# Performance work log

Measured on AMD Instinct MI355X. Metric: run time of the kernel, lower is better.

Reference implementation:

```python
import jax, jax.numpy as jnp
import numpy as np

EPS = 1e-5

def _silu(x):
    return x * jax.nn.sigmoid(x)

def _layernorm(x, g, b):
    mu = jnp.mean(x, axis=-1, keepdims=True)
    var = jnp.mean((x - mu) ** 2, axis=-1, keepdims=True)
    return (x - mu) * jax.lax.rsqrt(var + EPS) * g + b

def _mamba(x, in_w, conv_w, conv_b, xproj_w, dt_w, dt_b, A_log, Dp, out_w):
    # x: (B, L, dm); faithful mamba-ssm block: in_proj -> causal dwconv -> silu ->
    # x_proj -> softplus(dt_proj) -> selective scan -> gate -> out_proj
    B, L, dm = x.shape
    di, K = conv_w.shape          # d_inner, d_conv
    ds = A_log.shape[1]           # d_state
    dtr = dt_w.shape[1]           # dt_rank
    xz = x @ in_w.T               # (B, L, 2*di)
    xi, z = jnp.split(xz, 2, axis=-1)
    # causal depthwise conv1d (pad K-1 on the left), kernel unrolled (K=4)
    xpad = jnp.pad(xi, ((0, 0), (K - 1, 0), (0, 0)))
    xc = conv_b + sum(conv_w[:, k] * xpad[:, k:k + L, :] for k in range(K))
    xc = _silu(xc)                # (B, L, di)
    xdbl = xc @ xproj_w.T         # (B, L, dtr + 2*ds)
    dt, Bm, Cm = jnp.split(xdbl, [dtr, dtr + ds], axis=-1)
    delta = jax.nn.softplus(dt @ dt_w.T + dt_b)        # (B, L, di)
    A = -jnp.exp(A_log)                                # (di, ds)
    dA = jnp.exp(delta[..., None] * A)                 # (B, L, di, ds)
    dBu = delta[..., None] * Bm[:, :, None, :] * xc[..., None]
    def step(h, inp):
        dA_t, dBu_t, C_t = inp                         # (B,di,ds),(B,di,ds),(B,ds)
        h = dA_t * h + dBu_t
        y = jnp.einsum('bdn,bn->bd', h, C_t)
        return h, y
    h0 = jnp.zeros((B, di, ds), dtype=x.dtype)
    _, ys = jax.lax.scan(step, h0, (dA.transpose(1, 0, 2, 3),
                                    dBu.transpose(1, 0, 2, 3),
                                    Cm.transpose(1, 0, 2)))
    y = ys.transpose(1, 0, 2) + xc * Dp                # (B, L, di)
    y = y * _silu(z)
    return y @ out_w.T                                 # (B, L, dm)

def _forward(t1, t2, t3, t4, t5,
             m0_in_w, m0_conv_w, m0_conv_b, m0_xproj_w, m0_dt_w, m0_dt_b, m0_Alog, m0_D, m0_out_w,
             m1_in_w, m1_conv_w, m1_conv_b, m1_xproj_w, m1_dt_w, m1_dt_b, m1_Alog, m1_D, m1_out_w,
             norm_g, norm_b, proj_w, proj_b, norm1_g, norm1_b, proj1_w, proj1_b, skip_scale):
    B = t1.shape[0]
    flat = lambda t, c: t.reshape(B, c, -1).transpose(0, 2, 1)   # (B, N, C)
    f1, f2, f3, f4, f5 = flat(t1, 8), flat(t2, 16), flat(t3, 24), flat(t4, 32), flat(t5, 48)
    c1 = jnp.concatenate([f1[:, :, 0:8], f2[:, :, 0:8], f3[:, :, 0:8], f4[:, :, 0:8], f5[:, :, 0:8]], axis=1)   # (B,21824,8)
    c2 = jnp.concatenate([f2[:, :, 8:16], f3[:, :, 8:16], f4[:, :, 8:16], f5[:, :, 8:16]], axis=1)              # (B,5440,8)
    c3 = jnp.concatenate([f3[:, :, 16:24], f4[:, :, 16:24], f5[:, :, 16:24]], axis=1)                           # (B,1344,8)
    c4 = jnp.concatenate([f4[:, :, 24:32], f5[:, :, 24:32]], axis=1)                                            # (B,320,8)
    c5 = f5[:, :, 32:48]                                                                                        # (B,64,16)
    def block8(c):
        y = _mamba(c, m0_in_w, m0_conv_w, m0_conv_b, m0_xproj_w, m0_dt_w, m0_dt_b, m0_Alog, m0_D, m0_out_w)
        return _layernorm(y + skip_scale * c, norm_g, norm_b) @ proj_w.T + proj_b
    x1m, x2m, x3m, x4m = block8(c1), block8(c2), block8(c3), block8(c4)
    y5 = _mamba(c5, m1_in_w, m1_conv_w, m1_conv_b, m1_xproj_w, m1_dt_w, m1_dt_b, m1_Alog, m1_D, m1_out_w)
    x5m = _layernorm(y5 + skip_scale * c5, norm1_g, norm1_b) @ proj1_w.T + proj1_b
    a1 = x1m[:, 0:16384, :]
    a2 = jnp.concatenate([x1m[:, 16384:20480, :], x2m[:, 0:4096, :]], axis=2)
    a3 = jnp.concatenate([x1m[:, 20480:21504, :], x2m[:, 4096:5120, :], x3m[:, 0:1024, :]], axis=2)
    a4 = jnp.concatenate([x1m[:, 21504:21760, :], x2m[:, 5120:5376, :], x3m[:, 1024:1280, :], x4m[:, 0:256, :]], axis=2)
    a5 = jnp.concatenate([x1m[:, 21760:, :], x2m[:, 5376:, :], x3m[:, 1280:, :], x4m[:, 256:, :], x5m], axis=2)
    x1 = a1.transpose(0, 2, 1).reshape(B, 8, 128, 128)
    x2 = a2.transpose(0, 2, 1).reshape(B, 16, 64, 64)
    x3 = a3.transpose(0, 2, 1).reshape(B, 24, 32, 32)
    x4 = a4.transpose(0, 2, 1).reshape(B, 32, 16, 16)
    x5 = a5.transpose(0, 2, 1).reshape(B, 48, 8, 8)
    return (x1, x2, x3, x4, x5)

def setup_inputs() -> dict:
    key = jax.random.key(0)
    ks = iter(jax.random.split(key, 64))
    B = 8
    def n(shape, s=1.0):
        return jax.random.normal(next(ks), shape, dtype=jnp.float32) * s
    inp = {
        't1': n((B, 8, 128, 128)), 't2': n((B, 16, 64, 64)), 't3': n((B, 24, 32, 32)),
        't4': n((B, 32, 16, 16)), 't5': n((B, 48, 8, 8)),
    }
    def mamba_params(pfx, dm):
        di, ds, K, dtr = 2 * dm, 16, 4, 1  # expand=2, d_state=16, d_conv=4, dt_rank=ceil(dm/16)=1
        return {
            pfx + '_in_w': n((2 * di, dm), dm ** -0.5),
            pfx + '_conv_w': n((di, K), 0.3),
            pfx + '_conv_b': n((di,), 0.1),
            pfx + '_xproj_w': n((dtr + 2 * ds, di), di ** -0.5),
            pfx + '_dt_w': n((di, dtr), 1.0),
            pfx + '_dt_b': n((di,), 0.1) - 3.0,
            pfx + '_Alog': jnp.log(jnp.tile(jnp.arange(1.0, ds + 1.0, dtype=jnp.float32), (di, 1))),
            pfx + '_D': jnp.ones((di,), jnp.float32),
            pfx + '_out_w': n((dm, di), di ** -0.5),
        }
    inp.update(mamba_params('m0', 8))
    inp.update(mamba_params('m1', 16))
    inp.update({
        'norm_g': jnp.ones((8,), jnp.float32), 'norm_b': jnp.zeros((8,), jnp.float32),
        'proj_w': n((8, 8), 8 ** -0.5), 'proj_b': jnp.zeros((8,), jnp.float32),
        'norm1_g': jnp.ones((16,), jnp.float32), 'norm1_b': jnp.zeros((16,), jnp.float32),
        'proj1_w': n((16, 16), 16 ** -0.5), 'proj1_b': jnp.zeros((16,), jnp.float32),
        'skip_scale': jnp.ones((1,), jnp.float32),
    })
    return inp

def reference(t1, t2, t3, t4, t5,
              m0_in_w, m0_conv_w, m0_conv_b, m0_xproj_w, m0_dt_w, m0_dt_b, m0_Alog, m0_D, m0_out_w,
              m1_in_w, m1_conv_w, m1_conv_b, m1_xproj_w, m1_dt_w, m1_dt_b, m1_Alog, m1_D, m1_out_w,
              norm_g, norm_b, proj_w, proj_b, norm1_g, norm1_b, proj1_w, proj1_b, skip_scale):
    return _forward(t1, t2, t3, t4, t5,
                    m0_in_w, m0_conv_w, m0_conv_b, m0_xproj_w, m0_dt_w, m0_dt_b, m0_Alog, m0_D, m0_out_w,
                    m1_in_w, m1_conv_w, m1_conv_b, m1_xproj_w, m1_dt_w, m1_dt_b, m1_Alog, m1_D, m1_out_w,
                    norm_g, norm_b, proj_w, proj_b, norm1_g, norm1_b, proj1_w, proj1_b, skip_scale)
```

## Files before the change

### kernel.cpp

```cpp
#include <hip/hip_runtime.h>
#include <cmath>

#define SCH 128
#define SUB 32
#define NCB 228
#define NCHUNK 1824
#define NSUB 7296
#define LOG2E 1.442695041f
#define LN2F  0.6931471806f
#define EXP2F(x) __builtin_exp2f(x)
#define LOG2F(x) __builtin_log2f(x)
#define SW_IN 0
#define SW_CONVW 256
#define SW_CONVB 320
#define SW_XPROJ 336
#define SW_DTW 864
#define SW_DTB 880
#define SW_A 896
#define SW_D 1152
#define SW_OUTW 1168
#define SW_NG 1296
#define SW_NB 1304
#define SW_PW 1312
#define SW_PB 1376
#define SW_SKIP 1384
#define REC 1392
#define RSTR 25
#define GR_C 3200
#define GR_X8 4224
#define GRECW 4736
#define SMEMP1 4592
#define C3 4592
#define X83 5616
#define YOF 6128
#define V_IN 0
#define V_CONVW 1024
#define V_CONVB 1152
#define V_XPROJ 1184
#define V_DTW 2240
#define V_DTB 2272
#define V_A 2304
#define V_D 2816
#define V_OUTW 2848
#define V_NG 3360
#define V_NB 3376
#define V_PW 3392
#define V_PB 3648
#define V_SKIP 3664
#define V_XC 3668
#define V_DL 5780
#define V_BM 7892
#define V_CM 8916
#define SMEM3 9940

struct Params {
  const float *t0, *t1, *t2, *t3, *t4;
  const float *in_w0,*conv_w0,*conv_b0,*xproj0,*dtw0,*dtb0,*Alog0,*D0,*outw0;
  const float *in_w1,*conv_w1,*conv_b1,*xproj1,*dtw1,*dtb1,*Alog1,*D1,*outw1;
  const float *ng,*nb,*pw,*pb,*n1g,*n1b,*p1w,*p1b,*skip;
  float* out;
  float *hloc, *sumdelta, *grec;
};

__device__ __forceinline__ float softplusf(float x) {
  float t = EXP2F(-fabsf(x) * LOG2E);
  return fmaxf(x, 0.f) + LOG2F(1.f + t) * LN2F;
}
__device__ __forceinline__ float siluf(float x) { return x * (1.f / (1.f + __expf(-x))); }
__device__ __forceinline__ unsigned pk(float a, float b) {
  unsigned ua = __float_as_uint(a) + 0x8000u;
  unsigned ub = __float_as_uint(b) + 0x8000u;
  return (ua >> 16) | (ub & 0xFFFF0000u);
}
__device__ __forceinline__ float lo16(unsigned w) { return __uint_as_float(w << 16); }
__device__ __forceinline__ float hi16(unsigned w) { return __uint_as_float(w & 0xFFFF0000u); }

struct Loc { int k, pos, ch, hw, C; };

__device__ __forceinline__ Loc locate(int seq, int l) {
  Loc r;
  if (seq == 0) { r.ch = 0;
    if (l < 16384)      { r.k=0; r.pos=l;        r.hw=16384; r.C=8;  }
    else if (l < 20480) { r.k=1; r.pos=l-16384;  r.hw=4096;  r.C=16; }
    else if (l < 21504) { r.k=2; r.pos=l-20480;  r.hw=1024;  r.C=24; }
    else if (l < 21760) { r.k=3; r.pos=l-21504;  r.hw=256;   r.C=32; }
    else                { r.k=4; r.pos=l-21760;  r.hw=64;    r.C=48; }
  } else if (seq == 1) { r.ch = 8;
    if (l < 4096)       { r.k=1; r.pos=l;        r.hw=4096;  r.C=16; }
    else if (l < 5120)  { r.k=2; r.pos=l-4096;   r.hw=1024;  r.C=24; }
    else if (l < 5376)  { r.k=3; r.pos=l-5120;   r.hw=256;   r.C=32; }
    else                { r.k=4; r.pos=l-5376;   r.hw=64;    r.C=48; }
  } else if (seq == 2) { r.ch = 16;
    if (l < 1024)       { r.k=2; r.pos=l;        r.hw=1024;  r.C=24; }
    else if (l < 1280)  { r.k=3; r.pos=l-1024;   r.hw=256;   r.C=32; }
    else                { r.k=4; r.pos=l-1280;   r.hw=64;    r.C=48; }
  } else { r.ch = 24;
    if (l < 256)        { r.k=3; r.pos=l;        r.hw=256;   r.C=32; }
    else                { r.k=4; r.pos=l-256;    r.hw=64;    r.C=48; }
  }
  return r;
}

__device__ __forceinline__ const float* tsel(const Params& p, int k) {
  switch (k) { case 0: return p.t0; case 1: return p.t1; case 2: return p.t2;
               case 3: return p.t3; default: return p.t4; }
}
__device__ __forceinline__ int outbase(int k) {
  switch (k) { case 0: return 0; case 1: return 1048576; case 2: return 1572864;
               case 3: return 1769472; default: return 1835008; }
}

__device__ __forceinline__ void gather8(const Params& p, int b, int seq, int l, float* c) {
  Loc lc = locate(seq, l);
  const float* t = tsel(p, lc.k);
  int base = (b * lc.C + lc.ch) * lc.hw + lc.pos;
  #pragma unroll
  for (int j = 0; j < 8; ++j) c[j] = t[base + j * lc.hw];
}

__device__ __forceinline__ void decode_bid(int bid, int& b, int& seq, int& l0, int& Sa) {
  b = bid / NCB;
  int r = bid - b * NCB;
  int c, L;
  if (r < 171)      { seq = 0; c = r;       L = 21824; }
  else if (r < 214) { seq = 1; c = r - 171; L = 5440;  }
  else if (r < 225) { seq = 2; c = r - 214; L = 1344;  }
  else              { seq = 3; c = r - 225; L = 320;   }
  l0 = c * SCH;
  int rem = L - l0;
  Sa = rem < SCH ? rem : SCH;
}

__device__ void load_w0(const Params& p, float* s, int tid) {
  for (int i = tid; i < 256; i += 256) s[SW_IN + i] = p.in_w0[i];
  for (int i = tid; i < 64;  i += 256) s[SW_CONVW + i] = p.conv_w0[i];
  for (int i = tid; i < 16;  i += 256) s[SW_CONVB + i] = p.conv_b0[i];
  for (int i = tid; i < 528; i += 256) s[SW_XPROJ + i] = p.xproj0[i];
  for (int i = tid; i < 16;  i += 256) s[SW_DTW + i] = p.dtw0[i];
  for (int i = tid; i < 16;  i += 256) s[SW_DTB + i] = p.dtb0[i];
  for (int i = tid; i < 256; i += 256) s[SW_A + i] = -__expf(p.Alog0[i]) * LOG2E;
  for (int i = tid; i < 16;  i += 256) s[SW_D + i] = p.D0[i];
  for (int i = tid; i < 128; i += 256) s[SW_OUTW + i] = p.outw0[i];
  for (int i = tid; i < 8;   i += 256) s[SW_NG + i] = p.ng[i];
  for (int i = tid; i < 8;   i += 256) s[SW_NB + i] = p.nb[i];
  for (int i = tid; i < 64;  i += 256) s[SW_PW + i] = p.pw[i];
  for (int i = tid; i < 8;   i += 256) s[SW_PB + i] = p.pb[i];
  if (tid == 0) s[SW_SKIP] = p.skip[0];
}

__device__ __forceinline__ float dot16h(const float* w, int ch0, int cho,
                                        const float* a, const float* o) {
  float4 wa0 = *(const float4*)&w[ch0];
  float4 wa1 = *(const float4*)&w[ch0 + 4];
  float4 wb0 = *(const float4*)&w[cho];
  float4 wb1 = *(const float4*)&w[cho + 4];
  float r = wa0.x * a[0];
  r = fmaf(wa0.y, a[1], r); r = fmaf(wa0.z, a[2], r); r = fmaf(wa0.w, a[3], r);
  r = fmaf(wa1.x, a[4], r); r = fmaf(wa1.y, a[5], r);
  r = fmaf(wa1.z, a[6], r); r = fmaf(wa1.w, a[7], r);
  r = fmaf(wb0.x, o[0], r); r = fmaf(wb0.y, o[1], r);
  r = fmaf(wb0.z, o[2], r); r = fmaf(wb0.w, o[3], r);
  r = fmaf(wb1.x, o[4], r); r = fmaf(wb1.y, o[5], r);
  r = fmaf(wb1.z, o[6], r); r = fmaf(wb1.w, o[7], r);
  return r;
}

__global__ __launch_bounds__(256, 8) void k_pass1(Params p) {
  __shared__ float s[SMEMP1];
  int tid = threadIdx.x;
  int cid = blockIdx.x;
  int b, seq, l0, Sa;
  decode_bid(cid, b, seq, l0, Sa);
  int tok = tid >> 1, hf = tid & 1;
  int ch0 = hf * 8, cho = 8 - ch0;
  bool act = tok < Sa;
  bool grow = tok < Sa + 3;
  bool hrow = (Sa == SCH) && (tok >= SCH - 3);
  unsigned* gc = (unsigned*)(p.grec + (size_t)cid * GRECW);
  float x8[8], x8h[8];
  {
    int l = l0 - 3 + tok;
    if (grow && l >= 0) gather8(p, b, seq, l, x8);
    else {
      #pragma unroll
      for (int j = 0; j < 8; ++j) x8[j] = 0.f;
    }
  }
  if (hrow) gather8(p, b, seq, l0 + tok, x8h);
  load_w0(p, s, tid);
  if (hf == 0) {
    if (grow && tok >= 3) {
      uint4 v = make_uint4(pk(x8[0], x8[1]), pk(x8[2], x8[3]),
                           pk(x8[4], x8[5]), pk(x8[6], x8[7]));
      *(uint4*)&gc[GR_X8 + (tok - 3) * 4] = v;
    }
    if (hrow) {
      uint4 v = make_uint4(pk(x8h[0], x8h[1]), pk(x8h[2], x8h[3]),
                           pk(x8h[4], x8h[5]), pk(x8h[6], x8h[7]));
      *(uint4*)&gc[GR_X8 + tok * 4] = v;
    }
  }
  __syncthreads();
  if (grow) {
    #pragma unroll
    for (int ii = 0; ii < 8; ++ii) {
      int i = ch0 + ii;
      float4 wa = *(const float4*)&s[SW_IN + i * 8];
      float4 wb = *(const float4*)&s[SW_IN + i * 8 + 4];
      float a = wa.x * x8[0];
      a = fmaf(wa.y, x8[1], a); a = fmaf(wa.z, x8[2], a); a = fmaf(wa.w, x8[3], a);
      a = fmaf(wb.x, x8[4], a); a = fmaf(wb.y, x8[5], a);
      a = fmaf(wb.z, x8[6], a); a = fmaf(wb.w, x8[7], a);
      s[REC + tok * 17 + i] = a;
    }
  }
  if (hrow) {
    int r = tok + 3;
    #pragma unroll
    for (int ii = 0; ii < 8; ++ii) {
      int i = ch0 + ii;
      float4 wa = *(const float4*)&s[SW_IN + i * 8];
      float4 wb = *(const float4*)&s[SW_IN + i * 8 + 4];
      float a = wa.x * x8h[0];
      a = fmaf(wa.y, x8h[1], a); a = fmaf(wa.z, x8h[2], a); a = fmaf(wa.w, x8h[3], a);
      a = fmaf(wb.x, x8h[4], a); a = fmaf(wb.y, x8h[5], a);
      a = fmaf(wb.z, x8h[6], a); a = fmaf(wb.w, x8h[7], a);
      s[REC + r * 17 + i] = a;
    }
  }
  __syncthreads();
  float xc8[8], xco[8];
  float dt = 0.f;
  if (act) {
    #pragma unroll
    for (int ii = 0; ii < 8; ++ii) {
      int i = ch0 + ii;
      float4 cw = *(const float4*)&s[SW_CONVW + i * 4];
      float a = s[SW_CONVB + i];
      a = fmaf(cw.x, s[REC + (tok + 0) * 17 + i], a);
      a = fmaf(cw.y, s[REC + (tok + 1) * 17 + i], a);
      a = fmaf(cw.z, s[REC + (tok + 2) * 17 + i], a);
      a = fmaf(cw.w, s[REC + (tok + 3) * 17 + i], a);
      xc8[ii] = siluf(a);
    }
    #pragma unroll
    for (int ii = 0; ii < 8; ++ii) xco[ii] = __shfl_xor(xc8[ii], 1);
    dt = dot16h(&s[SW_XPROJ], ch0, cho, xc8, xco);
  }
  __syncthreads();
  unsigned* ru = (unsigned*)&s[REC + tok * RSTR];
  if (act) {
    #pragma unroll
    for (int q = 0; q < 4; ++q) {
      int d0 = ch0 + 2 * q;
      float da = softplusf(fmaf(dt, s[SW_DTW + d0],     s[SW_DTB + d0]));
      float db = softplusf(fmaf(dt, s[SW_DTW + d0 + 1], s[SW_DTB + d0 + 1]));
      ru[hf * 4 + q]     = pk(da, db);
      ru[8 + hf * 4 + q] = pk(xc8[2*q], xc8[2*q + 1]);
    }
    #pragma unroll
    for (int q = 0; q < 4; ++q) {
      int n0 = ch0 + 2 * q;
      float a0 = dot16h(&s[SW_XPROJ + (1 + n0) * 16], ch0, cho, xc8, xco);
      float a1 = dot16h(&s[SW_XPROJ + (2 + n0) * 16], ch0, cho, xc8, xco);
      ru[16 + hf * 4 + q] = pk(a0, a1);
    }
    uint4 cv;
    {
      int n0 = ch0;
      float a0 = dot16h(&s[SW_XPROJ + (17 + n0) * 16], ch0, cho, xc8, xco);
      float a1 = dot16h(&s[SW_XPROJ + (18 + n0) * 16], ch0, cho, xc8, xco);
      float a2 = dot16h(&s[SW_XPROJ + (19 + n0) * 16], ch0, cho, xc8, xco);
      float a3 = dot16h(&s[SW_XPROJ + (20 + n0) * 16], ch0, cho, xc8, xco);
      float a4 = dot16h(&s[SW_XPROJ + (21 + n0) * 16], ch0, cho, xc8, xco);
      float a5 = dot16h(&s[SW_XPROJ + (22 + n0) * 16], ch0, cho, xc8, xco);
      float a6 = dot16h(&s[SW_XPROJ + (23 + n0) * 16], ch0, cho, xc8, xco);
      float a7 = dot16h(&s[SW_XPROJ + (24 + n0) * 16], ch0, cho, xc8, xco);
      cv = make_uint4(pk(a0, a1), pk(a2, a3), pk(a4, a5), pk(a6, a7));
    }
    *(uint4*)&gc[GR_C + tok * 8 + hf * 4] = cv;
  } else {
    #pragma unroll
    for (int q = 0; q < 4; ++q) {
      ru[hf * 4 + q] = 0u;
      ru[8 + hf * 4 + q] = 0u;
      ru[16 + hf * 4 + q] = 0u;
    }
    *(uint4*)&gc[GR_C + tok * 8 + hf * 4] = make_uint4(0u, 0u, 0u, 0u);
  }
  __syncthreads();
  const unsigned* su = (const unsigned*)s;
  {
    uint4* g4 = (uint4*)gc;
    const uint4* s4 = (const uint4*)&su[REC];
    #pragma unroll 2
    for (int i4 = tid; i4 < GR_C / 4; i4 += 256) g4[i4] = s4[i4];
  }
  int w = tid >> 6, lane = tid & 63;
  int d = lane >> 2, ng = lane & 3;
  int dh = d >> 1;
  bool dodd = d & 1;
  int t0 = w * SUB;
  float4 Av = *(float4*)&s[SW_A + d * 16 + ng * 4];
  float h0 = 0.f, h1 = 0.f, h2 = 0.f, h3 = 0.f, sd = 0.f;
  for (int tile = 0; tile < 8; ++tile) {
    int tb = t0 + tile * 4;
    unsigned wd[4], wx[4]; uint2 wB[4];
    #pragma unroll
    for (int i = 0; i < 4; ++i) {
      int base = REC + (tb + i) * RSTR;
      wd[i] = su[base + dh];
      wx[i] = su[base + 8 + dh];
      wB[i] = *(const uint2*)&su[base + 16 + ng * 2];
    }
    #pragma unroll
    for (int i = 0; i < 4; ++i) {
      float dl = dodd ? hi16(wd[i]) : lo16(wd[i]);
      float u = dl * (dodd ? hi16(wx[i]) : lo16(wx[i]));
      float e0 = EXP2F(Av.x * dl), e1 = EXP2F(Av.y * dl);
      float e2 = EXP2F(Av.z * dl), e3 = EXP2F(Av.w * dl);
      h0 = fmaf(e0, h0, u * lo16(wB[i].x));
      h1 = fmaf(e1, h1, u * hi16(wB[i].x));
      h2 = fmaf(e2, h2, u * lo16(wB[i].y));
      h3 = fmaf(e3, h3, u * hi16(wB[i].y));
      sd += dl;
    }
  }
  int gs = cid * 4 + w;
  unsigned* hu = (unsigned*)p.hloc;
  hu[gs * 128 + d * 8 + ng * 2]     = pk(h0, h1);
  hu[gs * 128 + d * 8 + ng * 2 + 1] = pk(h2, h3);
  if (ng == 0) p.sumdelta[(size_t)gs * 16 + d] = sd;
}

__device__ void load_w1(const Params& p, float* s, int tid) {
  for (int i = tid; i < 1024; i += 256) s[V_IN + i] = p.in_w1[i];
  for (int i = tid; i < 128;  i += 256) s[V_CONVW + i] = p.conv_w1[i];
  for (int i = tid; i < 32;   i += 256) s[V_CONVB + i] = p.conv_b1[i];
  for (int i = tid; i < 1056; i += 256) s[V_XPROJ + i] = p.xproj1[i];
  for (int i = tid; i < 32;   i += 256) s[V_DTW + i] = p.dtw1[i];
  for (int i = tid; i < 32;   i += 256) s[V_DTB + i] = p.dtb1[i];
  for (int i = tid; i < 512;  i += 256) s[V_A + i] = -__expf(p.Alog1[i]) * LOG2E;
  for (int i = tid; i < 32;   i += 256) s[V_D + i] = p.D1[i];
  for (int i = tid; i < 512;  i += 256) s[V_OUTW + i] = p.outw1[i];
  for (int i = tid; i < 16;   i += 256) s[V_NG + i] = p.n1g[i];
  for (int i = tid; i < 16;   i += 256) s[V_NB + i] = p.n1b[i];
  for (int i = tid; i < 256;  i += 256) s[V_PW + i] = p.p1w[i];
  for (int i = tid; i < 16;   i += 256) s[V_PB + i] = p.p1b[i];
  if (tid == 0) s[V_SKIP] = p.skip[0];
}

__device__ void c5_path(const Params& p, float* s, int b, int tid) {
  load_w1(p, s, tid);
  int og = tid >> 6, tok = tid & 63;
  float x16[16];
  #pragma unroll
  for (int j = 0; j < 16; ++j) x16[j] = p.t4[(b * 48 + 32 + j) * 64 + tok];
  __syncthreads();
  #pragma unroll
  for (int ii = 0; ii < 8; ++ii) {
    int i = og * 8 + ii;
    float a = 0.f;
    #pragma unroll
    for (int j = 0; j < 16; ++j) a = fmaf(s[V_IN + i * 16 + j], x16[j], a);
    float xm1 = __shfl_up(a, 1);
    float xm2 = __shfl_up(a, 2);
    float xm3 = __shfl_up(a, 3);
    float c = s[V_CONVB + i];
    c = fmaf(s[V_CONVW + i * 4 + 3], a, c);
    if (tok >= 1) c = fmaf(s[V_CONVW + i * 4 + 2], xm1, c);
    if (tok >= 2) c = fmaf(s[V_CONVW + i * 4 + 1], xm2, c);
    if (tok >= 3) c = fmaf(s[V_CONVW + i * 4 + 0], xm3, c);
    s[V_XC + tok * 33 + i] = siluf(c);
  }
  __syncthreads();
  float xcr[32];
  #pragma unroll
  for (int i = 0; i < 32; ++i) xcr[i] = s[V_XC + tok * 33 + i];
  float dt = 0.f;
  #pragma unroll
  for (int i = 0; i < 32; ++i) dt = fmaf(s[V_XPROJ + i], xcr[i], dt);
  #pragma unroll
  for (int nn = 0; nn < 4; ++nn) {
    int n = og * 4 + nn;
    float aB = 0.f, aC = 0.f;
    #pragma unroll
    for (int i = 0; i < 32; ++i) {
      aB = fmaf(s[V_XPROJ + (1 + n) * 32 + i], xcr[i], aB);
      aC = fmaf(s[V_XPROJ + (17 + n) * 32 + i], xcr[i], aC);
    }
    s[V_BM + tok * 16 + n] = aB;
    s[V_CM + tok * 16 + n] = aC;
  }
  #pragma unroll
  for (int ii = 0; ii < 8; ++ii) {
    int d = og * 8 + ii;
    s[V_DL + tok * 33 + d] = softplusf(fmaf(dt, s[V_DTW + d], s[V_DTB + d]));
  }
  __syncthreads();
  if (tid < 128) {
    int d = tid >> 2, ng = tid & 3;
    float4 Av = *(float4*)&s[V_A + d * 16 + ng * 4];
    float h0 = 0.f, h1 = 0.f, h2 = 0.f, h3 = 0.f;
    for (int tile = 0; tile < 16; ++tile) {
      int tb = tile * 4;
      float dl[4], xv[4]; float4 bm[4], cm[4];
      #pragma unroll
      for (int i = 0; i < 4; ++i) {
        dl[i] = s[V_DL + (tb + i) * 33 + d];
        xv[i] = s[V_XC + (tb + i) * 33 + d];
        bm[i] = *(float4*)&s[V_BM + (tb + i) * 16 + ng * 4];
        cm[i] = *(float4*)&s[V_CM + (tb + i) * 16 + ng * 4];
      }
      float yp[4];
      #pragma unroll
      for (int i = 0; i < 4; ++i) {
        float u = dl[i] * xv[i];
        float e0 = EXP2F(Av.x * dl[i]), e1 = EXP2F(Av.y * dl[i]);
        float e2 = EXP2F(Av.z * dl[i]), e3 = EXP2F(Av.w * dl[i]);
        h0 = fmaf(e0, h0, u * bm[i].x);
        h1 = fmaf(e1, h1, u * bm[i].y);
        h2 = fmaf(e2, h2, u * bm[i].z);
        h3 = fmaf(e3, h3, u * bm[i].w);
        float y = h0 * cm[i].x;
        y = fmaf(h1, cm[i].y, y); y = fmaf(h2, cm[i].z, y); y = fmaf(h3, cm[i].w, y);
        yp[i] = y;
      }
      #pragma unroll
      for (int i = 0; i < 4; ++i) yp[i] += __shfl_xor(yp[i], 1);
      #pragma unroll
      for (int i = 0; i < 4; ++i) yp[i] += __shfl_xor(yp[i], 2);
      float ysel = ng == 0 ? yp[0] : ng == 1 ? yp[1] : ng == 2 ? yp[2] : yp[3];
      s[V_DL + (tb + ng) * 33 + d] = ysel;
    }
  }
  __syncthreads();
  #pragma unroll
  for (int ii = 0; ii < 8; ++ii) {
    int d = og * 8 + ii;
    float z = 0.f;
    #pragma unroll
    for (int j = 0; j < 16; ++j) z = fmaf(s[V_IN + (32 + d) * 16 + j], x16[j], z);
    float yv = (s[V_DL + tok * 33 + d] + s[V_XC + tok * 33 + d] * s[V_D + d]) * siluf(z);
    s[V_DL + tok * 33 + d] = yv;
  }
  __syncthreads();
  float yr[32];
  #pragma unroll
  for (int d = 0; d < 32; ++d) yr[d] = s[V_DL + tok * 33 + d];
  float sk = s[V_SKIP];
  #pragma unroll
  for (int mm = 0; mm < 4; ++mm) {
    int m = og * 4 + mm;
    float a = sk * x16[m];
    #pragma unroll
    for (int d = 0; d < 32; ++d) a = fmaf(s[V_OUTW + m * 32 + d], yr[d], a);
    s[V_XC + tok * 33 + m] = a;
  }
  __syncthreads();
  if (tid < 64) {
    float ov[16];
    #pragma unroll
    for (int m = 0; m < 16; ++m) ov[m] = s[V_XC + tok * 33 + m];
    float mu = 0.f;
    #pragma unroll
    for (int m = 0; m < 16; ++m) mu += ov[m];
    mu *= (1.f / 16.f);
    float var = 0.f;
    #pragma unroll
    for (int m = 0; m < 16; ++m) { float t = ov[m] - mu; var += t * t; }
    var *= (1.f / 16.f);
    float inv = rsqrtf(var + 1e-5f);
    #pragma unroll
    for (int m = 0; m < 16; ++m)
      s[V_XC + tok * 33 + m] = (ov[m] - mu) * inv * s[V_NG + m] + s[V_NB + m];
  }
  __syncthreads();
  float lr[16];
  #pragma unroll
  for (int j = 0; j < 16; ++j) lr[j] = s[V_XC + tok * 33 + j];
  #pragma unroll
  for (int mm = 0; mm < 4; ++mm) {
    int m = og * 4 + mm;
    float a = s[V_PB + m];
    #pragma unroll
    for (int j = 0; j < 16; ++j) a = fmaf(s[V_PW + m * 16 + j], lr[j], a);
    p.out[1835008 + (b * 48 + 32 + m) * 64 + tok] = a;
  }
}

__global__ __launch_bounds__(256) void k_pass2(Params p) {
  __shared__ unsigned sh[684 * 8];
  __shared__ float ssd[684];
  __shared__ float sS[32];
  __shared__ float sH[512];
  int bid = blockIdx.x, tid = threadIdx.x;
  int b = bid >> 6;
  int rr = bid & 63;
  int seq = rr >> 4, d = rr & 15;
  const int nch[4] = {171, 43, 11, 3};
  const int chf[4] = {0, 171, 214, 225};
  int nsub = nch[seq] * 4;
  int g0 = (b * NCB + chf[seq]) * 4;
  unsigned* hu = (unsigned*)p.hloc;
  int n8 = nsub * 8;
  for (int wdx = tid; wdx < n8; wdx += 256) {
    int rec = wdx >> 3, pr_ = wdx & 7;
    sh[wdx] = hu[(size_t)(g0 + rec) * 128 + d * 8 + pr_];
  }
  for (int rec = tid; rec < nsub; rec += 256)
    ssd[rec] = p.sumdelta[(size_t)(g0 + rec) * 16 + d];
  int g = tid >> 3, pr = tid & 7;
  float A0 = -__expf(p.Alog0[d * 16 + pr * 2]) * LOG2E;
  float A1 = -__expf(p.Alog0[d * 16 + pr * 2 + 1]) * LOG2E;
  __syncthreads();
  int T = (nsub + 31) >> 5;
  int i0 = g * T;
  int i1 = i0 + T; if (i1 > nsub) i1 = nsub;
  float S = 0.f, h0 = 0.f, h1 = 0.f;
  for (int i = i0; i < i1; ++i) {
    unsigned wl = sh[i * 8 + pr];
    float sv = ssd[i];
    float e0 = EXP2F(A0 * sv), e1 = EXP2F(A1 * sv);
    h0 = fmaf(e0, h0, lo16(wl));
    h1 = fmaf(e1, h1, hi16(wl));
    S += sv;
  }
  if (pr == 0) sS[g] = S;
  sH[g * 16 + pr * 2]     = h0;
  sH[g * 16 + pr * 2 + 1] = h1;
  __syncthreads();
  float q0 = 0.f, q1 = 0.f;
  for (int j = 0; j < g; ++j) {
    float Sj = sS[j];
    float e0 = EXP2F(A0 * Sj), e1 = EXP2F(A1 * Sj);
    q0 = fmaf(e0, q0, sH[j * 16 + pr * 2]);
    q1 = fmaf(e1, q1, sH[j * 16 + pr * 2 + 1]);
  }
  for (int i = i0; i < i1; ++i) {
    unsigned wl = sh[i * 8 + pr];
    float sv = ssd[i];
    sh[i * 8 + pr] = pk(q0, q1);
    float e0 = EXP2F(A0 * sv), e1 = EXP2F(A1 * sv);
    q0 = fmaf(e0, q0, lo16(wl));
    q1 = fmaf(e1, q1, hi16(wl));
  }
  __syncthreads();
  for (int wdx = tid; wdx < n8; wdx += 256) {
    int rec = wdx >> 3, pr_ = wdx & 7;
    hu[(size_t)(g0 + rec) * 128 + d * 8 + pr_] = sh[wdx];
  }
}

__global__ __launch_bounds__(256, 4) void k_pass3(Params p) {
  __shared__ float s[SMEM3];
  int tid = threadIdx.x;
  if (blockIdx.x < 8) { c5_path(p, s, blockIdx.x, tid); return; }
  load_w0(p, s, tid);
  int w = tid >> 6, lane = tid & 63;
  int d = lane >> 2, ng = lane & 3;
  int dh = d >> 1;
  bool dodd = d & 1;
  int t0 = w * SUB;
  int tok = tid >> 1, hf = tid & 1, ch0 = hf * 8;
  const unsigned* su = (const unsigned*)s;
  int cid = blockIdx.x - 8;
  int b, seq, l0, Sa;
  decode_bid(cid, b, seq, l0, Sa);
  {
    const uint4* g4 = (const uint4*)(p.grec + (size_t)cid * GRECW);
    uint4* s4 = (uint4*)&((unsigned*)s)[REC];
    #pragma unroll 2
    for (int i4 = tid; i4 < GRECW / 4; i4 += 256) s4[i4] = g4[i4];
  }
  __syncthreads();
  int gs = cid * 4 + w;
  float4 Av = *(float4*)&s[SW_A + d * 16 + ng * 4];
  const unsigned* hu = (const unsigned*)p.hloc;
  unsigned hw0 = hu[gs * 128 + d * 8 + ng * 2];
  unsigned hw1 = hu[gs * 128 + d * 8 + ng * 2 + 1];
  float h0 = lo16(hw0), h1 = hi16(hw0), h2 = lo16(hw1), h3 = hi16(hw1);
  for (int tile = 0; tile < 8; ++tile) {
    int tb = t0 + tile * 4;
    unsigned wd[4], wx[4]; uint2 wB[4], wC[4];
    #pragma unroll
    for (int i = 0; i < 4; ++i) {
      int base = REC + (tb + i) * RSTR;
      wd[i] = su[base + dh];
      wx[i] = su[base + 8 + dh];
      wB[i] = *(const uint2*)&su[base + 16 + ng * 2];
      wC[i] = *(const uint2*)&su[C3 + (tb + i) * 8 + ng * 2];
    }
    float yp[4];
    #pragma unroll
    for (int i = 0; i < 4; ++i) {
      float dl = dodd ? hi16(wd[i]) : lo16(wd[i]);
      float u = dl * (dodd ? hi16(wx[i]) : lo16(wx[i]));
      float e0 = EXP2F(Av.x * dl), e1 = EXP2F(Av.y * dl);
      float e2 = EXP2F(Av.z * dl), e3 = EXP2F(Av.w * dl);
      h0 = fmaf(e0, h0, u * lo16(wB[i].x));
      h1 = fmaf(e1, h1, u * hi16(wB[i].x));
      h2 = fmaf(e2, h2, u * lo16(wB[i].y));
      h3 = fmaf(e3, h3, u * hi16(wB[i].y));
      float y = h0 * lo16(wC[i].x);
      y = fmaf(h1, hi16(wC[i].x), y);
      y = fmaf(h2, lo16(wC[i].y), y);
      y = fmaf(h3, hi16(wC[i].y), y);
      yp[i] = y;
    }
    #pragma unroll
    for (int i = 0; i < 4; ++i) yp[i] += __shfl_xor(yp[i], 1);
    #pragma unroll
    for (int i = 0; i < 4; ++i) yp[i] += __shfl_xor(yp[i], 2);
    float ysel = ng == 0 ? yp[0] : ng == 1 ? yp[1] : ng == 2 ? yp[2] : yp[3];
    s[YOF + (tb + ng) * 17 + d] = ysel;
  }
  __syncthreads();
  if (tok < Sa) {
    const unsigned* xp = (const unsigned*)&s[X83 + tok * 4];
    float c8[8];
    #pragma unroll
    for (int q = 0; q < 4; ++q) { c8[2*q] = lo16(xp[q]); c8[2*q+1] = hi16(xp[q]); }
    const unsigned* ru = (const unsigned*)&s[REC + tok * RSTR];
    float yv8[8];
    #pragma unroll
    for (int q = 0; q < 4; ++q) {
      unsigned wv = ru[8 + hf * 4 + q];
      int d0 = ch0 + 2 * q;
      float4 w0a = *(const float4*)&s[SW_IN + (16 + d0) * 8];
      float4 w0b = *(const float4*)&s[SW_IN + (16 + d0) * 8 + 4];
      float4 w1a = *(const float4*)&s[SW_IN + (17 + d0) * 8];
      float4 w1b = *(const float4*)&s[SW_IN + (17 + d0) * 8 + 4];
      float z0 = w0a.x * c8[0];
      z0 = fmaf(w0a.y, c8[1], z0); z0 = fmaf(w0a.z, c8[2], z0); z0 = fmaf(w0a.w, c8[3], z0);
      z0 = fmaf(w0b.x, c8[4], z0); z0 = fmaf(w0b.y, c8[5], z0);
      z0 = fmaf(w0b.z, c8[6], z0); z0 = fmaf(w0b.w, c8[7], z0);
      float z1 = w1a.x * c8[0];
      z1 = fmaf(w1a.y, c8[1], z1); z1 = fmaf(w1a.z, c8[2], z1); z1 = fmaf(w1a.w, c8[3], z1);
      z1 = fmaf(w1b.x, c8[4], z1); z1 = fmaf(w1b.y, c8[5], z1);
      z1 = fmaf(w1b.z, c8[6], z1); z1 = fmaf(w1b.w, c8[7], z1);
      yv8[2*q]   = (s[YOF + tok * 17 + d0]     + lo16(wv) * s[SW_D + d0])     * siluf(z0);
      yv8[2*q+1] = (s[YOF + tok * 17 + d0 + 1] + hi16(wv) * s[SW_D + d0 + 1]) * siluf(z1);
    }
    float o[8];
    float sk = s[SW_SKIP];
    #pragma unroll
    for (int m = 0; m < 8; ++m) {
      float4 wv0 = *(const float4*)&s[SW_OUTW + m * 16 + ch0];
      float4 wv1 = *(const float4*)&s[SW_OUTW + m * 16 + ch0 + 4];
      float a = wv0.x * yv8[0];
      a = fmaf(wv0.y, yv8[1], a); a = fmaf(wv0.z, yv8[2], a); a = fmaf(wv0.w, yv8[3], a);
      a = fmaf(wv1.x, yv8[4], a); a = fmaf(wv1.y, yv8[5], a);
      a = fmaf(wv1.z, yv8[6], a); a = fmaf(wv1.w, yv8[7], a);
      a += __shfl_xor(a, 1);
      o[m] = a + sk * c8[m];
    }
    float mu = 0.f;
    #pragma unroll
    for (int m = 0; m < 8; ++m) mu += o[m];
    mu *= 0.125f;
    float var = 0.f;
    #pragma unroll
    for (int m = 0; m < 8; ++m) { float t = o[m] - mu; var += t * t; }
    var *= 0.125f;
    float inv = rsqrtf(var + 1e-5f);
    #pragma unroll
    for (int m = 0; m < 8; ++m) o[m] = (o[m] - mu) * inv * s[SW_NG + m] + s[SW_NB + m];
    Loc lc = locate(seq, l0 + tok);
    int obase = outbase(lc.k) + (b * lc.C + lc.ch) * lc.hw + lc.pos;
    #pragma unroll
    for (int mm = 0; mm < 4; ++mm) {
      int m = hf * 4 + mm;
      float4 pw0 = *(const float4*)&s[SW_PW + m * 8];
      float4 pw1 = *(const float4*)&s[SW_PW + m * 8 + 4];
      float a = s[SW_PB + m];
      a = fmaf(pw0.x, o[0], a); a = fmaf(pw0.y, o[1], a);
      a = fmaf(pw0.z, o[2], a); a = fmaf(pw0.w, o[3], a);
      a = fmaf(pw1.x, o[4], a); a = fmaf(pw1.y, o[5], a);
      a = fmaf(pw1.z, o[6], a); a = fmaf(pw1.w, o[7], a);
      p.out[obase + m * lc.hw] = a;
    }
  }
}

extern "C" void kernel_launch(void* const* d_in, const int* in_sizes, int n_in,
                              void* d_out, int out_size, void* d_ws, size_t ws_size,
                              hipStream_t stream) {
  (void)in_sizes; (void)n_in; (void)out_size; (void)ws_size;
  Params p;
  p.t0 = (const float*)d_in[0];  p.t1 = (const float*)d_in[1];
  p.t2 = (const float*)d_in[2];  p.t3 = (const float*)d_in[3];
  p.t4 = (const float*)d_in[4];
  p.in_w0   = (const float*)d_in[5];
  p.conv_w0 = (const float*)d_in[6];
  p.conv_b0 = (const float*)d_in[7];
  p.xproj0  = (const float*)d_in[8];
  p.dtw0    = (const float*)d_in[9];
  p.dtb0    = (const float*)d_in[10];
  p.Alog0   = (const float*)d_in[11];
  p.D0      = (const float*)d_in[12];
  p.outw0   = (const float*)d_in[13];
  p.in_w1   = (const float*)d_in[14];
  p.conv_w1 = (const float*)d_in[15];
  p.conv_b1 = (const float*)d_in[16];
  p.xproj1  = (const float*)d_in[17];
  p.dtw1    = (const float*)d_in[18];
  p.dtb1    = (const float*)d_in[19];
  p.Alog1   = (const float*)d_in[20];
  p.D1      = (const float*)d_in[21];
  p.outw1   = (const float*)d_in[22];
  p.ng  = (const float*)d_in[23];
  p.nb  = (const float*)d_in[24];
  p.pw  = (const float*)d_in[25];
  p.pb  = (const float*)d_in[26];
  p.n1g = (const float*)d_in[27];
  p.n1b = (const float*)d_in[28];
  p.p1w = (const float*)d_in[29];
  p.p1b = (const float*)d_in[30];
  p.skip = (const float*)d_in[31];
  p.out = (float*)d_out;
  float* ws = (float*)d_ws;
  p.hloc     = ws;
  p.sumdelta = ws + (size_t)NSUB * 128;
  p.grec     = ws + (size_t)NSUB * 128 + (size_t)NSUB * 16;
  k_pass1<<<dim3(NCHUNK), dim3(256), 0, stream>>>(p);
  k_pass2<<<dim3(512), dim3(256), 0, stream>>>(p);
  k_pass3<<<dim3(NCHUNK + 8), dim3(256), 0, stream>>>(p);
}
```

Baseline: 113.9 us.

## Replace inter-chunk scan pass with per-chunk aggregates and serial prefix in pass3

Removes the separate pass2 kernel that propagated SSM states across chunks. Pass1 now also writes a per-chunk aggregate (summed delta and combined state) to a workspace buffer. Pass3 then computes each chunk's incoming state by serially folding all preceding chunk aggregates in the same sequence. This drops one kernel launch and a global round trip, but the serial loop can run up to about 170 iterations for long sequences, which adds latency and imbalance for later chunks.

```diff
diff --git a/kernel.cpp b/kernel.cpp
--- a/kernel.cpp
+++ b/kernel.cpp
@@ -24,6 +24,8 @@
 #define SW_PW 1312
 #define SW_PB 1376
 #define SW_SKIP 1384
+#define PSCR_H 256
+#define PSCR_S 768
 #define REC 1392
 #define RSTR 25
 #define GR_C 3200
@@ -33,6 +35,7 @@
 #define C3 4592
 #define X83 5616
 #define YOF 6128
+#define AGGW 160
 #define V_IN 0
 #define V_CONVW 1024
 #define V_CONVB 1152
@@ -59,7 +62,7 @@
   const float *in_w1,*conv_w1,*conv_b1,*xproj1,*dtw1,*dtb1,*Alog1,*D1,*outw1;
   const float *ng,*nb,*pw,*pb,*n1g,*n1b,*p1w,*p1b,*skip;
   float* out;
-  float *hloc, *sumdelta, *grec;
+  float *hloc, *sumdelta, *grec, *agg;
 };
 
 __device__ __forceinline__ float softplusf(float x) {
@@ -167,6 +170,7 @@
 
 __global__ __launch_bounds__(256, 8) void k_pass1(Params p) {
   __shared__ float s[SMEMP1];
+  unsigned* su32 = (unsigned*)s;
   int tid = threadIdx.x;
   int cid = blockIdx.x;
   int b, seq, l0, Sa;
@@ -248,7 +252,7 @@
     dt = dot16h(&s[SW_XPROJ], ch0, cho, xc8, xco);
   }
   __syncthreads();
-  unsigned* ru = (unsigned*)&s[REC + tok * RSTR];
+  unsigned* ru = &su32[REC + tok * RSTR];
   if (act) {
     #pragma unroll
     for (int q = 0; q < 4; ++q) {
@@ -267,15 +271,14 @@
     }
     uint4 cv;
     {
-      int n0 = ch0;
-      float a0 = dot16h(&s[SW_XPROJ + (17 + n0) * 16], ch0, cho, xc8, xco);
-      float a1 = dot16h(&s[SW_XPROJ + (18 + n0) * 16], ch0, cho, xc8, xco);
-      float a2 = dot16h(&s[SW_XPROJ + (19 + n0) * 16], ch0, cho, xc8, xco);
-      float a3 = dot16h(&s[SW_XPROJ + (20 + n0) * 16], ch0, cho, xc8, xco);
-      float a4 = dot16h(&s[SW_XPROJ + (21 + n0) * 16], ch0, cho, xc8, xco);
-      float a5 = dot16h(&s[SW_XPROJ + (22 + n0) * 16], ch0, cho, xc8, xco);
-      float a6 = dot16h(&s[SW_XPROJ + (23 + n0) * 16], ch0, cho, xc8, xco);
-      float a7 = dot16h(&s[SW_XPROJ + (24 + n0) * 16], ch0, cho, xc8, xco);
+      float a0 = dot16h(&s[SW_XPROJ + (17 + ch0) * 16], ch0, cho, xc8, xco);
+      float a1 = dot16h(&s[SW_XPROJ + (18 + ch0) * 16], ch0, cho, xc8, xco);
+      float a2 = dot16h(&s[SW_XPROJ + (19 + ch0) * 16], ch0, cho, xc8, xco);
+      float a3 = dot16h(&s[SW_XPROJ + (20 + ch0) * 16], ch0, cho, xc8, xco);
+      float a4 = dot16h(&s[SW_XPROJ + (21 + ch0) * 16], ch0, cho, xc8, xco);
+      float a5 = dot16h(&s[SW_XPROJ + (22 + ch0) * 16], ch0, cho, xc8, xco);
+      float a6 = dot16h(&s[SW_XPROJ + (23 + ch0) * 16], ch0, cho, xc8, xco);
+      float a7 = dot16h(&s[SW_XPROJ + (24 + ch0) * 16], ch0, cho, xc8, xco);
       cv = make_uint4(pk(a0, a1), pk(a2, a3), pk(a4, a5), pk(a6, a7));
     }
     *(uint4*)&gc[GR_C + tok * 8 + hf * 4] = cv;
@@ -289,10 +292,9 @@
     *(uint4*)&gc[GR_C + tok * 8 + hf * 4] = make_uint4(0u, 0u, 0u, 0u);
   }
   __syncthreads();
-  const unsigned* su = (const unsigned*)s;
   {
     uint4* g4 = (uint4*)gc;
-    const uint4* s4 = (const uint4*)&su[REC];
+    const uint4* s4 = (const uint4*)&su32[REC];
     #pragma unroll 2
     for (int i4 = tid; i4 < GR_C / 4; i4 += 256) g4[i4] = s4[i4];
   }
@@ -309,9 +311,9 @@
     #pragma unroll
     for (int i = 0; i < 4; ++i) {
       int base = REC + (tb + i) * RSTR;
-      wd[i] = su[base + dh];
-      wx[i] = su[base + 8 + dh];
-      wB[i] = *(const uint2*)&su[base + 16 + ng * 2];
+      wd[i] = su32[base + dh];
+      wx[i] = su32[base + 8 + dh];
+      wB[i] = *(const uint2*)&su32[base + 16 + ng * 2];
     }
     #pragma unroll
     for (int i = 0; i < 4; ++i) {
@@ -328,9 +330,31 @@
   }
   int gs = cid * 4 + w;
   unsigned* hu = (unsigned*)p.hloc;
-  hu[gs * 128 + d * 8 + ng * 2]     = pk(h0, h1);
-  hu[gs * 128 + d * 8 + ng * 2 + 1] = pk(h2, h3);
+  unsigned hp01 = pk(h0, h1), hp23 = pk(h2, h3);
+  hu[gs * 128 + d * 8 + ng * 2]     = hp01;
+  hu[gs * 128 + d * 8 + ng * 2 + 1] = hp23;
   if (ng == 0) p.sumdelta[(size_t)gs * 16 + d] = sd;
+  su32[PSCR_H + w * 128 + d * 8 + ng * 2]     = hp01;
+  su32[PSCR_H + w * 128 + d * 8 + ng * 2 + 1] = hp23;
+  if (ng == 0) s[PSCR_S + w * 16 + d] = sd;
+  __syncthreads();
+  if (tid < 128) {
+    int dd = tid >> 3, pr = tid & 7;
+    float A0 = s[SW_A + dd * 16 + pr * 2];
+    float A1 = s[SW_A + dd * 16 + pr * 2 + 1];
+    float Sag = 0.f, hA0 = 0.f, hA1 = 0.f;
+    #pragma unroll
+    for (int w_ = 0; w_ < 4; ++w_) {
+      unsigned lw = su32[PSCR_H + w_ * 128 + dd * 8 + pr];
+      float sw = s[PSCR_S + w_ * 16 + dd];
+      float e0 = EXP2F(A0 * sw), e1 = EXP2F(A1 * sw);
+      hA0 = fmaf(e0, hA0, lo16(lw));
+      hA1 = fmaf(e1, hA1, hi16(lw));
+      Sag += sw;
+    }
+    ((unsigned*)p.agg)[(size_t)cid * AGGW + 16 + dd * 8 + pr] = pk(hA0, hA1);
+    if (pr == 0) p.agg[(size_t)cid * AGGW + dd] = Sag;
+  }
 }
 
 __device__ void load_w1(const Params& p, float* s, int tid) {
@@ -489,71 +513,9 @@
   }
 }
 
-__global__ __launch_bounds__(256) void k_pass2(Params p) {
-  __shared__ unsigned sh[684 * 8];
-  __shared__ float ssd[684];
-  __shared__ float sS[32];
-  __shared__ float sH[512];
-  int bid = blockIdx.x, tid = threadIdx.x;
-  int b = bid >> 6;
-  int rr = bid & 63;
-  int seq = rr >> 4, d = rr & 15;
-  const int nch[4] = {171, 43, 11, 3};
-  const int chf[4] = {0, 171, 214, 225};
-  int nsub = nch[seq] * 4;
-  int g0 = (b * NCB + chf[seq]) * 4;
-  unsigned* hu = (unsigned*)p.hloc;
-  int n8 = nsub * 8;
-  for (int wdx = tid; wdx < n8; wdx += 256) {
-    int rec = wdx >> 3, pr_ = wdx & 7;
-    sh[wdx] = hu[(size_t)(g0 + rec) * 128 + d * 8 + pr_];
-  }
-  for (int rec = tid; rec < nsub; rec += 256)
-    ssd[rec] = p.sumdelta[(size_t)(g0 + rec) * 16 + d];
-  int g = tid >> 3, pr = tid & 7;
-  float A0 = -__expf(p.Alog0[d * 16 + pr * 2]) * LOG2E;
-  float A1 = -__expf(p.Alog0[d * 16 + pr * 2 + 1]) * LOG2E;
-  __syncthreads();
-  int T = (nsub + 31) >> 5;
-  int i0 = g * T;
-  int i1 = i0 + T; if (i1 > nsub) i1 = nsub;
-  float S = 0.f, h0 = 0.f, h1 = 0.f;
-  for (int i = i0; i < i1; ++i) {
-    unsigned wl = sh[i * 8 + pr];
-    float sv = ssd[i];
-    float e0 = EXP2F(A0 * sv), e1 = EXP2F(A1 * sv);
-    h0 = fmaf(e0, h0, lo16(wl));
-    h1 = fmaf(e1, h1, hi16(wl));
-    S += sv;
-  }
-  if (pr == 0) sS[g] = S;
-  sH[g * 16 + pr * 2]     = h0;
-  sH[g * 16 + pr * 2 + 1] = h1;
-  __syncthreads();
-  float q0 = 0.f, q1 = 0.f;
-  for (int j = 0; j < g; ++j) {
-    float Sj = sS[j];
-    float e0 = EXP2F(A0 * Sj), e1 = EXP2F(A1 * Sj);
-    q0 = fmaf(e0, q0, sH[j * 16 + pr * 2]);
-    q1 = fmaf(e1, q1, sH[j * 16 + pr * 2 + 1]);
-  }
-  for (int i = i0; i < i1; ++i) {
-    unsigned wl = sh[i * 8 + pr];
-    float sv = ssd[i];
-    sh[i * 8 + pr] = pk(q0, q1);
-    float e0 = EXP2F(A0 * sv), e1 = EXP2F(A1 * sv);
-    q0 = fmaf(e0, q0, lo16(wl));
-    q1 = fmaf(e1, q1, hi16(wl));
-  }
-  __syncthreads();
-  for (int wdx = tid; wdx < n8; wdx += 256) {
-    int rec = wdx >> 3, pr_ = wdx & 7;
-    hu[(size_t)(g0 + rec) * 128 + d * 8 + pr_] = sh[wdx];
-  }
-}
-
 __global__ __launch_bounds__(256, 4) void k_pass3(Params p) {
   __shared__ float s[SMEM3];
+  unsigned* su32 = (unsigned*)s;
   int tid = threadIdx.x;
   if (blockIdx.x < 8) { c5_path(p, s, blockIdx.x, tid); return; }
   load_w0(p, s, tid);
@@ -563,22 +525,48 @@
   bool dodd = d & 1;
   int t0 = w * SUB;
   int tok = tid >> 1, hf = tid & 1, ch0 = hf * 8;
-  const unsigned* su = (const unsigned*)s;
   int cid = blockIdx.x - 8;
   int b, seq, l0, Sa;
   decode_bid(cid, b, seq, l0, Sa);
   {
     const uint4* g4 = (const uint4*)(p.grec + (size_t)cid * GRECW);
-    uint4* s4 = (uint4*)&((unsigned*)s)[REC];
+    uint4* s4 = (uint4*)&su32[REC];
     #pragma unroll 2
     for (int i4 = tid; i4 < GRECW / 4; i4 += 256) s4[i4] = g4[i4];
   }
   __syncthreads();
-  int gs = cid * 4 + w;
+  {
+    const int chf_[4] = {0, 171, 214, 225};
+    int c0 = b * NCB + chf_[seq];
+    if (tid < 128) {
+      int dd = tid >> 3, pr = tid & 7;
+      float A0 = s[SW_A + dd * 16 + pr * 2];
+      float A1 = s[SW_A + dd * 16 + pr * 2 + 1];
+      float hp0 = 0.f, hp1 = 0.f;
+      for (int j = c0; j < cid; ++j) {
+        float sv = p.agg[(size_t)j * AGGW + dd];
+        unsigned hw = ((const unsigned*)p.agg)[(size_t)j * AGGW + 16 + dd * 8 + pr];
+        float e0 = EXP2F(A0 * sv), e1 = EXP2F(A1 * sv);
+        hp0 = fmaf(e0, hp0, lo16(hw));
+        hp1 = fmaf(e1, hp1, hi16(hw));
+      }
+      const unsigned* hu = (const unsigned*)p.hloc;
+      #pragma unroll
+      for (int w_ = 0; w_ < 4; ++w_) {
+        int gs = cid * 4 + w_;
+        unsigned lw = hu[(size_t)gs * 128 + dd * 8 + pr];
+        float sw = p.sumdelta[(size_t)gs * 16 + dd];
+        su32[PSCR_H + w_ * 128 + dd * 8 + pr] = pk(hp0, hp1);
+        float e0 = EXP2F(A0 * sw), e1 = EXP2F(A1 * sw);
+        hp0 = fmaf(e0, hp0, lo16(lw));
+        hp1 = fmaf(e1, hp1, hi16(lw));
+      }
+    }
+  }
+  __syncthreads();
   float4 Av = *(float4*)&s[SW_A + d * 16 + ng * 4];
-  const unsigned* hu = (const unsigned*)p.hloc;
-  unsigned hw0 = hu[gs * 128 + d * 8 + ng * 2];
-  unsigned hw1 = hu[gs * 128 + d * 8 + ng * 2 + 1];
+  unsigned hw0 = su32[PSCR_H + w * 128 + d * 8 + ng * 2];
+  unsigned hw1 = su32[PSCR_H + w * 128 + d * 8 + ng * 2 + 1];
   float h0 = lo16(hw0), h1 = hi16(hw0), h2 = lo16(hw1), h3 = hi16(hw1);
   for (int tile = 0; tile < 8; ++tile) {
     int tb = t0 + tile * 4;
@@ -586,10 +574,10 @@
     #pragma unroll
     for (int i = 0; i < 4; ++i) {
       int base = REC + (tb + i) * RSTR;
-      wd[i] = su[base + dh];
-      wx[i] = su[base + 8 + dh];
-      wB[i] = *(const uint2*)&su[base + 16 + ng * 2];
-      wC[i] = *(const uint2*)&su[C3 + (tb + i) * 8 + ng * 2];
+      wd[i] = su32[base + dh];
+      wx[i] = su32[base + 8 + dh];
+      wB[i] = *(const uint2*)&su32[base + 16 + ng * 2];
+      wC[i] = *(const uint2*)&su32[C3 + (tb + i) * 8 + ng * 2];
     }
     float yp[4];
     #pragma unroll
@@ -617,11 +605,11 @@
   }
   __syncthreads();
   if (tok < Sa) {
-    const unsigned* xp = (const unsigned*)&s[X83 + tok * 4];
+    const unsigned* xp = &su32[X83 + tok * 4];
     float c8[8];
     #pragma unroll
     for (int q = 0; q < 4; ++q) { c8[2*q] = lo16(xp[q]); c8[2*q+1] = hi16(xp[q]); }
-    const unsigned* ru = (const unsigned*)&s[REC + tok * RSTR];
+    const unsigned* ru = &su32[REC + tok * RSTR];
     float yv8[8];
     #pragma unroll
     for (int q = 0; q < 4; ++q) {
@@ -723,7 +711,7 @@
   p.hloc     = ws;
   p.sumdelta = ws + (size_t)NSUB * 128;
   p.grec     = ws + (size_t)NSUB * 128 + (size_t)NSUB * 16;
+  p.agg      = p.grec + (size_t)NCHUNK * GRECW;
   k_pass1<<<dim3(NCHUNK), dim3(256), 0, stream>>>(p);
-  k_pass2<<<dim3(512), dim3(256), 0, stream>>>(p);
   k_pass3<<<dim3(NCHUNK + 8), dim3(256), 0, stream>>>(p);
 }
```

Measured after the change: 146.4 us. 1.28x slower.
